# Kernel tuning notes

Hardware: AMD Instinct MI355X
Metric: run time of the kernel (lower is better)

## Reference

```python
import jax, jax.numpy as jnp
import numpy as np
import math

H = 128  # hidden_dim
RADIUS = 30.0


def _lin(x, w, b):
    return x @ w + b


def _masked_softmax(logits, mask):
    return jax.nn.softmax(jnp.where(mask, logits, -1e9), axis=-1)


def setup_inputs() -> dict:
    key = jax.random.key(0)
    ks = iter(jax.random.split(key, 64))

    def p(shape, s=0.02):
        return (jax.random.normal(next(ks), shape, jnp.float32) * s)

    B, N, T, M, L = 2, 48, 24, 192, 20
    inp = {
        'agents_state': jax.random.normal(next(ks), (B, N, T, 5), jnp.float32),
        'agents_mask': jnp.ones((B, N, T), jnp.float32),
        'map_polylines': jax.random.normal(next(ks), (B, M, L, 2), jnp.float32),
        'map_poly_mask': jnp.ones((B, M), jnp.float32),
        'map_poly_type': jax.random.randint(next(ks), (B, M), 0, 4),
        'map_tl_status': jax.random.randint(next(ks), (B, M), 0, 8),
        'map_on_route': jax.random.randint(next(ks), (B, M), 0, 2),
        # AgentStateEncoder
        'ae_w0': p((5, H)), 'ae_b0': p((H,)), 'ae_w1': p((H, H)), 'ae_b1': p((H,)),
        'ae_w2': p((H, H)), 'ae_b2': p((H,)),
        # MapPolylineNodeEncoder point_mlp
        'mp_w0': p((2, H)), 'mp_b0': p((H,)), 'mp_w1': p((H, H)), 'mp_b1': p((H,)),
        'type_emb': p((4, H)), 'tl_emb': p((8, H)), 'route_emb': p((2, H)),
        'mo_w0': p((H, H)), 'mo_b0': p((H,)), 'mo_w1': p((H, H)), 'mo_b1': p((H,)),
        # map_rel_mlp (3 -> H -> 1)
        'mr_w0': p((3, H)), 'mr_b0': p((H,)), 'mr_w1': p((H, 1)), 'mr_b1': p((1,)),
        # nbr_rel_mlp (5 -> H -> 1)
        'nr_w0': p((5, H)), 'nr_b0': p((H,)), 'nr_w1': p((H, 1)), 'nr_b1': p((1,)),
        # tau_out (3H -> H -> 64)
        'to_w0': p((3 * H, H)), 'to_b0': p((H,)), 'to_w1': p((H, 64)), 'to_b1': p((64,)),
    }
    return inp


def reference(agents_state, agents_mask, map_polylines, map_poly_mask,
              map_poly_type, map_tl_status, map_on_route,
              ae_w0, ae_b0, ae_w1, ae_b1, ae_w2, ae_b2,
              mp_w0, mp_b0, mp_w1, mp_b1, type_emb, tl_emb, route_emb,
              mo_w0, mo_b0, mo_w1, mo_b1,
              mr_w0, mr_b0, mr_w1, mr_b1,
              nr_w0, nr_b0, nr_w1, nr_b1,
              to_w0, to_b0, to_w1, to_b1):
    B, N, T, _ = agents_state.shape
    a_mask = agents_mask > 0.5
    a_feat = agents_state[..., :5]

    # --- MapPolylineNodeEncoder ---
    m = map_poly_mask > 0.5
    h = jax.nn.relu(_lin(jax.nn.relu(_lin(map_polylines, mp_w0, mp_b0)), mp_w1, mp_b1))  # B,M,L,H
    h = h.max(axis=2)  # B,M,H
    pt = jnp.clip(map_poly_type, 0, type_emb.shape[0] - 1)
    tl = jnp.clip(map_tl_status, 0, tl_emb.shape[0] - 1)
    rt = jnp.clip(map_on_route, 0, route_emb.shape[0] - 1)
    h = h + type_emb[pt] + tl_emb[tl] + route_emb[rt]
    h = _lin(jax.nn.relu(_lin(h, mo_w0, mo_b0)), mo_w1, mo_b1)
    map_node = h * m[..., None].astype(h.dtype)  # B,M,D
    map_center = map_polylines.mean(axis=2)  # B,M,2

    # --- AgentStateEncoder ---
    a = jax.nn.relu(_lin(a_feat, ae_w0, ae_b0))
    a = jax.nn.relu(_lin(a, ae_w1, ae_b1))
    a_emb = _lin(a, ae_w2, ae_b2) * a_mask[..., None].astype(a.dtype)  # B,N,T,D

    # --- map cross-attention with relative-position bias ---
    agent_pos = a_feat[..., 0:2]
    rel = map_center[:, None, None, :, :] - agent_pos[:, :, :, None, :]  # B,N,T,M,2
    dist = jnp.linalg.norm(rel, axis=-1, keepdims=True)
    rel_feat = jnp.concatenate([rel, dist], axis=-1)  # B,N,T,M,3
    rel_score = _lin(jax.nn.relu(_lin(rel_feat, mr_w0, mr_b0)), mr_w1, mr_b1)[..., 0]  # B,N,T,M
    dot = jnp.einsum('bntd,bmd->bntm', a_emb, map_node) / math.sqrt(map_node.shape[-1])
    attn = _masked_softmax(dot + rel_score, m[:, None, None, :])
    map_ctx = jnp.einsum('bntm,bmd->bntd', attn, map_node)

    # --- neighbor graph attention ---
    pos = a_feat[..., 0:2]
    vel = a_feat[..., 3:5]
    rel_pos = jnp.transpose(pos[:, :, None] - pos[:, None, :], (0, 1, 3, 2, 4))  # B,N,T,N,2
    rel_vel = jnp.transpose(vel[:, :, None] - vel[:, None, :], (0, 1, 3, 2, 4))
    dist_ij = jnp.linalg.norm(rel_pos, axis=-1, keepdims=True)  # B,N,T,N,1
    rel_ij = jnp.concatenate([rel_pos, rel_vel, dist_ij], axis=-1)  # B,N,T,N,5
    nbr_score = _lin(jax.nn.relu(_lin(rel_ij, nr_w0, nr_b0)), nr_w1, nr_b1)[..., 0]  # B,N,T,N

    valid_i = a_mask[..., None]  # B,N,T,1
    valid_j = jnp.transpose(a_mask, (0, 2, 1))[:, None, :, :]  # B,1,T,N
    radius_ok = dist_ij[..., 0] <= RADIUS
    not_self = ~jnp.eye(N, dtype=bool)[None, :, None, :]  # 1,N,1,N
    nbr_mask = valid_i & valid_j & radius_ok & not_self

    dot_n = jnp.einsum('bntd,bjtd->bntj', a_emb, a_emb) / math.sqrt(a_emb.shape[-1])
    w_n = _masked_softmax(dot_n + nbr_score, nbr_mask)  # B,N,T,N
    nbr_ctx = jnp.einsum('bntj,bjtd->bntd', w_n, a_emb)

    tau = jnp.concatenate([a_emb, map_ctx, nbr_ctx], axis=-1)
    tau = _lin(jax.nn.relu(_lin(tau, to_w0, to_b0)), to_w1, to_b1)
    tau = tau * a_mask[..., None].astype(tau.dtype)
    return tau, map_ctx, nbr_ctx
```

## Files before the change

kernel.cpp:

```cpp
#include <hip/hip_runtime.h>
#include <math.h>

#define HH 128
#define BB 2
#define NN 48
#define TT 24
#define MM 192
#define LL 20
#define NT (BB*NN*TT)
#define RSQRT_H 0.08838834764831845f
#define RADIUS_C 30.0f

struct P {
    const float *astate, *amask, *polylines, *poly_mask;
    const int *ptype, *tlst, *route;
    const float *ae_w0,*ae_b0,*ae_w1,*ae_b1,*ae_w2,*ae_b2;
    const float *mp_w0,*mp_b0,*mp_w1,*mp_b1;
    const float *type_emb,*tl_emb,*route_emb;
    const float *mo_w0,*mo_b0,*mo_w1,*mo_b1;
    const float *mr_w0,*mr_b0,*mr_w1,*mr_b1;
    const float *nr_w0,*nr_b0,*nr_w1,*nr_b1;
    const float *to_w0,*to_b0,*to_w1,*to_b1;
    float *tau,*map_ctx,*nbr_ctx;
    float *a_emb,*map_node,*map_nodeT,*map_center;
};

struct SME { float pts[LL*2]; float h1[LL][HH]; float mx[2][HH]; float hb[HH]; float pr[2][HH]; float hb2[HH]; };
struct SAG { float xin[4][5]; float h1[4][HH]; float h2[4][HH]; float p1[2][4][HH]; };

struct SF {
    float4 aq4L[HH];
    float  mctx[4][HH];
    float  nctx[4][HH];
    float  pc[2][4][HH];
    union {
        struct {
            float  mnL[16][MM];
            float4 w4L[HH];
            float  w1L[HH];
            float  lg[4][MM];
            float4 p4L[MM];
            float  invL[4];
        } m;
        struct {
            float  pjL[NN][8];
            float4 wAL[HH];
            float4 wBL[HH];
            float  sPL[4][4][NN];
            float  dPL[4][4][NN];
            float  lgN[4][NN];
            float4 pN[NN];
        } n;
        struct {
            float  xinT[3*HH][4];
            float  h1T[HH][4];
        } t;
    } u;
};

__device__ void do_map_enc(const P& p, SME& s, int bm) {
    int tid = threadIdx.x, pp = tid >> 7, c = tid & 127;
    if (tid < LL*2) s.pts[tid] = p.polylines[(size_t)bm*LL*2 + tid];
    __syncthreads();
    {
        float w0x = p.mp_w0[c], w0y = p.mp_w0[HH + c], b0 = p.mp_b0[c];
        #pragma unroll
        for (int i = 0; i < 10; ++i) {
            int pt_ = pp + 2*i;
            s.h1[pt_][c] = fmaxf(fmaf(s.pts[2*pt_], w0x, fmaf(s.pts[2*pt_+1], w0y, b0)), 0.f);
        }
    }
    if (tid < 2) {
        float sum = 0.f;
        for (int q = 0; q < LL; ++q) sum += s.pts[2*q + tid];
        p.map_center[bm*2 + tid] = sum * (1.0f / LL);
    }
    __syncthreads();
    {
        float acc[10];
        float b1 = p.mp_b1[c];
        #pragma unroll
        for (int i = 0; i < 10; ++i) acc[i] = b1;
        for (int k = 0; k < HH; ++k) {
            float wv = p.mp_w1[k*HH + c];
            #pragma unroll
            for (int i = 0; i < 10; ++i) acc[i] = fmaf(s.h1[pp + 2*i][k], wv, acc[i]);
        }
        float m10 = acc[0];
        #pragma unroll
        for (int i = 1; i < 10; ++i) m10 = fmaxf(m10, acc[i]);
        s.mx[pp][c] = m10;
    }
    __syncthreads();
    if (tid < HH) {
        float hm = fmaxf(fmaxf(s.mx[0][c], s.mx[1][c]), 0.f);
        int pt = p.ptype[bm]; pt = pt < 0 ? 0 : (pt > 3 ? 3 : pt);
        int tv = p.tlst[bm];  tv = tv < 0 ? 0 : (tv > 7 ? 7 : tv);
        int rv = p.route[bm]; rv = rv < 0 ? 0 : (rv > 1 ? 1 : rv);
        hm += p.type_emb[pt*HH + c] + p.tl_emb[tv*HH + c] + p.route_emb[rv*HH + c];
        s.hb[c] = hm;
    }
    __syncthreads();
    {
        float sum = 0.f;
        int k0 = pp*64;
        for (int k = k0; k < k0 + 64; ++k) sum = fmaf(s.hb[k], p.mo_w0[k*HH + c], sum);
        s.pr[pp][c] = sum;
    }
    __syncthreads();
    if (tid < HH) s.hb2[c] = fmaxf(s.pr[0][c] + s.pr[1][c] + p.mo_b0[c], 0.f);
    __syncthreads();
    {
        float sum = 0.f;
        int k0 = pp*64;
        for (int k = k0; k < k0 + 64; ++k) sum = fmaf(s.hb2[k], p.mo_w1[k*HH + c], sum);
        s.pr[pp][c] = sum;
    }
    __syncthreads();
    if (tid < HH) {
        float a3 = s.pr[0][c] + s.pr[1][c] + p.mo_b1[c];
        float mk = (p.poly_mask[bm] > 0.5f) ? 1.f : 0.f;
        float v = a3 * mk;
        p.map_node[(size_t)bm*HH + c] = v;
        int b = bm / MM, m = bm % MM;
        p.map_nodeT[((size_t)b*HH + c)*MM + m] = v;
    }
}

__device__ void do_agent_enc(const P& p, SAG& s, int r0) {
    int tid = threadIdx.x, h = tid >> 7, c = tid & 127;
    if (tid < 20) s.xin[tid/5][tid%5] = p.astate[(size_t)r0*5 + tid];
    __syncthreads();
    if (h == 0) {
        float b = p.ae_b0[c];
        float w[5];
        #pragma unroll
        for (int i = 0; i < 5; ++i) w[i] = p.ae_w0[i*HH + c];
        #pragma unroll
        for (int r = 0; r < 4; ++r) {
            float v = b;
            #pragma unroll
            for (int i = 0; i < 5; ++i) v = fmaf(s.xin[r][i], w[i], v);
            s.h1[r][c] = fmaxf(v, 0.f);
        }
    }
    __syncthreads();
    {
        float acc[4] = {0.f,0.f,0.f,0.f};
        int k0 = h*64;
        for (int k = k0; k < k0 + 64; ++k) {
            float wv = p.ae_w1[k*HH + c];
            #pragma unroll
            for (int r = 0; r < 4; ++r) acc[r] = fmaf(s.h1[r][k], wv, acc[r]);
        }
        #pragma unroll
        for (int r = 0; r < 4; ++r) s.p1[h][r][c] = acc[r];
    }
    __syncthreads();
    {
        #pragma unroll
        for (int rr = 0; rr < 2; ++rr) {
            int r = h*2 + rr;
            s.h2[r][c] = fmaxf(s.p1[0][r][c] + s.p1[1][r][c] + p.ae_b1[c], 0.f);
        }
    }
    __syncthreads();
    {
        float acc[4] = {0.f,0.f,0.f,0.f};
        int k0 = h*64;
        for (int k = k0; k < k0 + 64; ++k) {
            float wv = p.ae_w2[k*HH + c];
            #pragma unroll
            for (int r = 0; r < 4; ++r) acc[r] = fmaf(s.h2[r][k], wv, acc[r]);
        }
        #pragma unroll
        for (int r = 0; r < 4; ++r) s.p1[h][r][c] = acc[r];
    }
    __syncthreads();
    {
        #pragma unroll
        for (int rr = 0; rr < 2; ++rr) {
            int r = h*2 + rr;
            int row = r0 + r;
            p.a_emb[(size_t)row*HH + c] = (s.p1[0][r][c] + s.p1[1][r][c] + p.ae_b2[c]) * p.amask[row];
        }
    }
}

__global__ __launch_bounds__(256) void k_enc(P p) {
    __shared__ __align__(16) char smraw[(sizeof(SME) > sizeof(SAG)) ? sizeof(SME) : sizeof(SAG)];
    int task = blockIdx.x;
    if (task < BB*MM) do_map_enc(p, *(SME*)smraw, task);
    else              do_agent_enc(p, *(SAG*)smraw, (task - BB*MM)*4);
}

__global__ __launch_bounds__(256) void k_fat(P p) {
    __shared__ __align__(16) SF s;
    int task = blockIdx.x;
    int b    = task / (TT*12);
    int rem  = task % (TT*12);
    int t    = rem / 12;
    int n0   = (rem % 12) * 4;
    int tid  = threadIdx.x;

    int row0 = (b*NN + n0)*TT + t;

    for (int idx = tid; idx < 4*HH; idx += 256) {
        int r = idx >> 7, k = idx & 127;
        ((float*)&s.aq4L[k])[r] = p.a_emb[(size_t)(row0 + r*TT)*HH + k];
    }
    if (tid < HH) {
        int k = tid;
        s.u.m.w4L[k] = make_float4(p.mr_w0[k], p.mr_w0[HH+k], p.mr_w0[2*HH+k], p.mr_b0[k]);
        s.u.m.w1L[k] = p.mr_w1[k];
    }

    float rx[4], ry[4], rd[4];
    if (tid < MM) {
        float mcx = p.map_center[(b*MM + tid)*2];
        float mcy = p.map_center[(b*MM + tid)*2 + 1];
        #pragma unroll
        for (int r = 0; r < 4; ++r) {
            float px = p.astate[(size_t)(row0 + r*TT)*5];
            float py = p.astate[(size_t)(row0 + r*TT)*5 + 1];
            rx[r] = mcx - px; ry[r] = mcy - py;
            rd[r] = sqrtf(rx[r]*rx[r] + ry[r]*ry[r]);
        }
    }

    const float* mnT = p.map_nodeT + (size_t)b*HH*MM;
    float4 st[3];
    #pragma unroll
    for (int i = 0; i < 3; ++i) {
        int q = tid + 256*i;
        int kk = q / 48, mq = q % 48;
        st[i] = *(const float4*)(mnT + (size_t)kk*MM + mq*4);
    }
    float sacc[4] = {0.f,0.f,0.f,0.f};
    float dt4[4]  = {0.f,0.f,0.f,0.f};
    for (int ch = 0; ch < 8; ++ch) {
        __syncthreads();
        #pragma unroll
        for (int i = 0; i < 3; ++i) {
            int q = tid + 256*i;
            int kk = q / 48, mq = q % 48;
            *(float4*)&s.u.m.mnL[kk][mq*4] = st[i];
        }
        __syncthreads();
        if (ch < 7) {
            #pragma unroll
            for (int i = 0; i < 3; ++i) {
                int q = tid + 256*i;
                int kk = q / 48, mq = q % 48;
                st[i] = *(const float4*)(mnT + (size_t)(ch+1)*16*MM + (size_t)kk*MM + mq*4);
            }
        }
        if (tid < MM) {
            int k0 = ch*16;
            #pragma unroll
            for (int kk = 0; kk < 16; ++kk) {
                int k = k0 + kk;
                float4 w  = s.u.m.w4L[k];
                float  w1 = s.u.m.w1L[k];
                float4 aq = s.aq4L[k];
                float  mn = s.u.m.mnL[kk][tid];
                #pragma unroll
                for (int r = 0; r < 4; ++r) {
                    float hv = fmaf(rx[r], w.x, fmaf(ry[r], w.y, fmaf(rd[r], w.z, w.w)));
                    sacc[r] = fmaf(fmaxf(hv, 0.f), w1, sacc[r]);
                }
                dt4[0] = fmaf(aq.x, mn, dt4[0]);
                dt4[1] = fmaf(aq.y, mn, dt4[1]);
                dt4[2] = fmaf(aq.z, mn, dt4[2]);
                dt4[3] = fmaf(aq.w, mn, dt4[3]);
            }
        }
    }
    if (tid < MM) {
        float pm = p.poly_mask[b*MM + tid];
        float b1 = p.mr_b1[0];
        #pragma unroll
        for (int r = 0; r < 4; ++r) {
            float lgt = fmaf(dt4[r], RSQRT_H, sacc[r] + b1);
            s.u.m.lg[r][tid] = (pm > 0.5f) ? lgt : -1e9f;
        }
    }
    __syncthreads();

    {
        int r = tid >> 6, l = tid & 63;
        float v = fmaxf(fmaxf(s.u.m.lg[r][l], s.u.m.lg[r][l+64]), s.u.m.lg[r][l+128]);
        #pragma unroll
        for (int o = 32; o > 0; o >>= 1) v = fmaxf(v, __shfl_xor(v, o));
        float e0 = expf(s.u.m.lg[r][l] - v);
        float e1 = expf(s.u.m.lg[r][l+64] - v);
        float e2 = expf(s.u.m.lg[r][l+128] - v);
        s.u.m.lg[r][l] = e0; s.u.m.lg[r][l+64] = e1; s.u.m.lg[r][l+128] = e2;
        float sm = e0 + e1 + e2;
        #pragma unroll
        for (int o = 32; o > 0; o >>= 1) sm += __shfl_xor(sm, o);
        if (l == 0) s.u.m.invL[r] = 1.0f / sm;
    }
    __syncthreads();
    if (tid < MM) {
        s.u.m.p4L[tid] = make_float4(s.u.m.lg[0][tid]*s.u.m.invL[0], s.u.m.lg[1][tid]*s.u.m.invL[1],
                                     s.u.m.lg[2][tid]*s.u.m.invL[2], s.u.m.lg[3][tid]*s.u.m.invL[3]);
    }
    __syncthreads();

    {
        int half = tid >> 7, c = tid & 127;
        float a0=0.f, a1=0.f, a2=0.f, a3=0.f;
        const float* mnb = p.map_node + ((size_t)b*MM + half*96)*HH + c;
        for (int m = 0; m < 96; ++m) {
            float mv = mnb[(size_t)m*HH];
            float4 pp4 = s.u.m.p4L[half*96 + m];
            a0 = fmaf(pp4.x, mv, a0); a1 = fmaf(pp4.y, mv, a1);
            a2 = fmaf(pp4.z, mv, a2); a3 = fmaf(pp4.w, mv, a3);
        }
        s.pc[half][0][c]=a0; s.pc[half][1][c]=a1; s.pc[half][2][c]=a2; s.pc[half][3][c]=a3;
    }
    __syncthreads();
    for (int idx = tid; idx < 4*HH; idx += 256) {
        int r = idx >> 7, c = idx & 127;
        float v = s.pc[0][r][c] + s.pc[1][r][c];
        s.mctx[r][c] = v;
        p.map_ctx[(size_t)(row0 + r*TT)*HH + c] = v;
    }
    __syncthreads();

    if (tid < NN) {
        int rj = (b*NN + tid)*TT + t;
        s.u.n.pjL[tid][0] = p.astate[(size_t)rj*5];
        s.u.n.pjL[tid][1] = p.astate[(size_t)rj*5 + 1];
        s.u.n.pjL[tid][2] = p.astate[(size_t)rj*5 + 3];
        s.u.n.pjL[tid][3] = p.astate[(size_t)rj*5 + 4];
        s.u.n.pjL[tid][4] = p.amask[rj];
    }
    if (tid < HH) {
        int k = tid;
        s.u.n.wAL[k] = make_float4(p.nr_w0[k], p.nr_w0[HH+k], p.nr_w0[2*HH+k], p.nr_w0[3*HH+k]);
        s.u.n.wBL[k] = make_float4(p.nr_w0[4*HH+k], p.nr_b0[k], p.nr_w1[k], 0.f);
    }
    __syncthreads();

    {
        int j  = tid % 48;
        int kg = tid / 48;
        if (kg < 4) {
            float jx = s.u.n.pjL[j][0], jy = s.u.n.pjL[j][1];
            float jvx = s.u.n.pjL[j][2], jvy = s.u.n.pjL[j][3];
            float dx[4], dy[4], dvx[4], dvy[4], dd[4];
            #pragma unroll
            for (int r = 0; r < 4; ++r) {
                int ni = n0 + r;
                dx[r]  = s.u.n.pjL[ni][0] - jx;  dy[r]  = s.u.n.pjL[ni][1] - jy;
                dvx[r] = s.u.n.pjL[ni][2] - jvx; dvy[r] = s.u.n.pjL[ni][3] - jvy;
                dd[r]  = sqrtf(dx[r]*dx[r] + dy[r]*dy[r]);
            }
            const float* aj = p.a_emb + ((size_t)(b*NN + j)*TT + t)*HH;
            float sr[4]  = {0,0,0,0};
            float dtn[4] = {0,0,0,0};
            int k0 = kg*32;
            for (int kk = 0; kk < 32; ++kk) {
                int k = k0 + kk;
                float4 wa = s.u.n.wAL[k], wb = s.u.n.wBL[k];
                float4 aq = s.aq4L[k];
                float  av = aj[k];
                #pragma unroll
                for (int r = 0; r < 4; ++r) {
                    float hv = fmaf(dx[r], wa.x, fmaf(dy[r], wa.y,
                               fmaf(dvx[r], wa.z, fmaf(dvy[r], wa.w,
                               fmaf(dd[r], wb.x, wb.y)))));
                    sr[r] = fmaf(fmaxf(hv, 0.f), wb.z, sr[r]);
                }
                dtn[0] = fmaf(aq.x, av, dtn[0]); dtn[1] = fmaf(aq.y, av, dtn[1]);
                dtn[2] = fmaf(aq.z, av, dtn[2]); dtn[3] = fmaf(aq.w, av, dtn[3]);
            }
            #pragma unroll
            for (int r = 0; r < 4; ++r) { s.u.n.sPL[kg][r][j] = sr[r]; s.u.n.dPL[kg][r][j] = dtn[r]; }
        }
    }
    __syncthreads();

    {
        float b1 = p.nr_b1[0];
        for (int idx = tid; idx < 4*NN; idx += 256) {
            int r = idx / NN, jj = idx % NN;
            int ni = n0 + r;
            float ss  = s.u.n.sPL[0][r][jj] + s.u.n.sPL[1][r][jj] + s.u.n.sPL[2][r][jj] + s.u.n.sPL[3][r][jj] + b1;
            float do2 = s.u.n.dPL[0][r][jj] + s.u.n.dPL[1][r][jj] + s.u.n.dPL[2][r][jj] + s.u.n.dPL[3][r][jj];
            float ddx = s.u.n.pjL[ni][0] - s.u.n.pjL[jj][0];
            float ddy = s.u.n.pjL[ni][1] - s.u.n.pjL[jj][1];
            float dist = sqrtf(ddx*ddx + ddy*ddy);
            bool ok = (s.u.n.pjL[ni][4] > 0.5f) && (s.u.n.pjL[jj][4] > 0.5f) &&
                      (dist <= RADIUS_C) && (jj != ni);
            s.u.n.lgN[r][jj] = ok ? fmaf(do2, RSQRT_H, ss) : -1e9f;
        }
    }
    __syncthreads();

    {
        int r = tid >> 6, l = tid & 63;
        float v = (l < NN) ? s.u.n.lgN[r][l] : -3.4e38f;
        #pragma unroll
        for (int o = 32; o > 0; o >>= 1) v = fmaxf(v, __shfl_xor(v, o));
        float e = (l < NN) ? expf(s.u.n.lgN[r][l] - v) : 0.f;
        float sm = e;
        #pragma unroll
        for (int o = 32; o > 0; o >>= 1) sm += __shfl_xor(sm, o);
        if (l < NN) s.u.n.lgN[r][l] = e / sm;
    }
    __syncthreads();
    if (tid < NN) {
        s.u.n.pN[tid] = make_float4(s.u.n.lgN[0][tid], s.u.n.lgN[1][tid],
                                    s.u.n.lgN[2][tid], s.u.n.lgN[3][tid]);
    }
    __syncthreads();

    {
        int half = tid >> 7, c = tid & 127;
        float a0=0.f, a1=0.f, a2=0.f, a3=0.f;
        for (int jj = half*24; jj < half*24 + 24; ++jj) {
            float av = p.a_emb[((size_t)(b*NN + jj)*TT + t)*HH + c];
            float4 pp4 = s.u.n.pN[jj];
            a0 = fmaf(pp4.x, av, a0); a1 = fmaf(pp4.y, av, a1);
            a2 = fmaf(pp4.z, av, a2); a3 = fmaf(pp4.w, av, a3);
        }
        s.pc[half][0][c]=a0; s.pc[half][1][c]=a1; s.pc[half][2][c]=a2; s.pc[half][3][c]=a3;
    }
    __syncthreads();
    for (int idx = tid; idx < 4*HH; idx += 256) {
        int r = idx >> 7, c = idx & 127;
        float v = s.pc[0][r][c] + s.pc[1][r][c];
        s.nctx[r][c] = v;
        p.nbr_ctx[(size_t)(row0 + r*TT)*HH + c] = v;
    }
    __syncthreads();

    for (int idx = tid; idx < 4*HH; idx += 256) {
        int r = idx >> 7, k = idx & 127;
        s.u.t.xinT[k][r]        = ((float*)&s.aq4L[k])[r];
        s.u.t.xinT[HH + k][r]   = s.mctx[r][k];
        s.u.t.xinT[2*HH + k][r] = s.nctx[r][k];
    }
    __syncthreads();
    {
        int c = tid & 127, h = tid >> 7;
        float acc[4] = {0,0,0,0};
        for (int k = h*192; k < h*192 + 192; ++k) {
            float wv = p.to_w0[k*HH + c];
            float4 xa = *(const float4*)&s.u.t.xinT[k][0];
            acc[0]=fmaf(xa.x,wv,acc[0]); acc[1]=fmaf(xa.y,wv,acc[1]);
            acc[2]=fmaf(xa.z,wv,acc[2]); acc[3]=fmaf(xa.w,wv,acc[3]);
        }
        #pragma unroll
        for (int r = 0; r < 4; ++r) s.pc[h][r][c] = acc[r];
    }
    __syncthreads();
    for (int idx = tid; idx < 4*HH; idx += 256) {
        int r = idx >> 7, k = idx & 127;
        s.u.t.h1T[k][r] = fmaxf(s.pc[0][r][k] + s.pc[1][r][k] + p.to_b0[k], 0.f);
    }
    __syncthreads();
    {
        int r = tid >> 6, c2 = tid & 63;
        float acc = p.to_b1[c2];
        for (int k = 0; k < HH; ++k)
            acc = fmaf(s.u.t.h1T[k][r], p.to_w1[k*64 + c2], acc);
        p.tau[(size_t)(row0 + r*TT)*64 + c2] = acc * p.amask[row0 + r*TT];
    }
}

extern "C" void kernel_launch(void* const* d_in, const int* in_sizes, int n_in,
                              void* d_out, int out_size, void* d_ws, size_t ws_size,
                              hipStream_t stream)
{
    P p;
    p.astate    = (const float*)d_in[0];
    p.amask     = (const float*)d_in[1];
    p.polylines = (const float*)d_in[2];
    p.poly_mask = (const float*)d_in[3];
    p.ptype     = (const int*)d_in[4];
    p.tlst      = (const int*)d_in[5];
    p.route     = (const int*)d_in[6];
    p.ae_w0 = (const float*)d_in[7];  p.ae_b0 = (const float*)d_in[8];
    p.ae_w1 = (const float*)d_in[9];  p.ae_b1 = (const float*)d_in[10];
    p.ae_w2 = (const float*)d_in[11]; p.ae_b2 = (const float*)d_in[12];
    p.mp_w0 = (const float*)d_in[13]; p.mp_b0 = (const float*)d_in[14];
    p.mp_w1 = (const float*)d_in[15]; p.mp_b1 = (const float*)d_in[16];
    p.type_emb  = (const float*)d_in[17];
    p.tl_emb    = (const float*)d_in[18];
    p.route_emb = (const float*)d_in[19];
    p.mo_w0 = (const float*)d_in[20]; p.mo_b0 = (const float*)d_in[21];
    p.mo_w1 = (const float*)d_in[22]; p.mo_b1 = (const float*)d_in[23];
    p.mr_w0 = (const float*)d_in[24]; p.mr_b0 = (const float*)d_in[25];
    p.mr_w1 = (const float*)d_in[26]; p.mr_b1 = (const float*)d_in[27];
    p.nr_w0 = (const float*)d_in[28]; p.nr_b0 = (const float*)d_in[29];
    p.nr_w1 = (const float*)d_in[30]; p.nr_b1 = (const float*)d_in[31];
    p.to_w0 = (const float*)d_in[32]; p.to_b0 = (const float*)d_in[33];
    p.to_w1 = (const float*)d_in[34]; p.to_b1 = (const float*)d_in[35];

    p.tau     = (float*)d_out;
    p.map_ctx = (float*)d_out + (size_t)NT*64;
    p.nbr_ctx = p.map_ctx + (size_t)NT*HH;

    float* ws    = (float*)d_ws;
    p.a_emb      = ws;
    p.map_node   = p.a_emb + (size_t)NT*HH;
    p.map_nodeT  = p.map_node + (size_t)BB*MM*HH;
    p.map_center = p.map_nodeT + (size_t)BB*MM*HH;

    k_enc<<<BB*MM + NT/4, 256, 0, stream>>>(p);
    k_fat<<<BB*TT*12,     256, 0, stream>>>(p);
}
```

Measured before the change: 187.9 us.

## Split agent encoder to two rows per block and simplify map-score and output stages

Agent encoding now handles two rows per block instead of four, doubling the block count. The map MLP's hidden buffer is transposed so each thread reads contiguous points. The map-attention loop drops its staged LDS copy of map_nodeT and reads coalesced columns straight from global memory, which removes eight barriers. The tau stage now splits the K dimension across both thread halves for two of its rows, while the other two rows run serially. Together these trade extra blocks and global reads for fewer barriers and more parallelism, though the uneven tau tail and the uncached global reads could offset some of that.

```diff
diff --git a/kernel.cpp b/kernel.cpp
--- a/kernel.cpp
+++ b/kernel.cpp
@@ -25,8 +25,8 @@
     float *a_emb,*map_node,*map_nodeT,*map_center;
 };
 
-struct SME { float pts[LL*2]; float h1[LL][HH]; float mx[2][HH]; float hb[HH]; float pr[2][HH]; float hb2[HH]; };
-struct SAG { float xin[4][5]; float h1[4][HH]; float h2[4][HH]; float p1[2][4][HH]; };
+struct SME { float pts[LL*2]; float h1T[HH][LL]; float mx[2][HH]; float hb[HH]; float pr[2][HH]; float hb2[HH]; };
+struct SAG { float xin[2][5]; float h1[2][HH]; float h2[2][HH]; float p1[2][2][HH]; };
 
 struct SF {
     float4 aq4L[HH];
@@ -35,7 +35,6 @@
     float  pc[2][4][HH];
     union {
         struct {
-            float  mnL[16][MM];
             float4 w4L[HH];
             float  w1L[HH];
             float  lg[4][MM];
@@ -52,8 +51,8 @@
             float4 pN[NN];
         } n;
         struct {
-            float  xinT[3*HH][4];
-            float  h1T[HH][4];
+            float4 xinT[3*HH];
+            float4 h1T[HH];
         } t;
     } u;
 };
@@ -66,8 +65,8 @@
         float w0x = p.mp_w0[c], w0y = p.mp_w0[HH + c], b0 = p.mp_b0[c];
         #pragma unroll
         for (int i = 0; i < 10; ++i) {
-            int pt_ = pp + 2*i;
-            s.h1[pt_][c] = fmaxf(fmaf(s.pts[2*pt_], w0x, fmaf(s.pts[2*pt_+1], w0y, b0)), 0.f);
+            int pt_ = pp*10 + i;
+            s.h1T[c][pt_] = fmaxf(fmaf(s.pts[2*pt_], w0x, fmaf(s.pts[2*pt_+1], w0y, b0)), 0.f);
         }
     }
     if (tid < 2) {
@@ -83,8 +82,9 @@
         for (int i = 0; i < 10; ++i) acc[i] = b1;
         for (int k = 0; k < HH; ++k) {
             float wv = p.mp_w1[k*HH + c];
+            const float* hrow = &s.h1T[k][pp*10];
             #pragma unroll
-            for (int i = 0; i < 10; ++i) acc[i] = fmaf(s.h1[pp + 2*i][k], wv, acc[i]);
+            for (int i = 0; i < 10; ++i) acc[i] = fmaf(hrow[i], wv, acc[i]);
         }
         float m10 = acc[0];
         #pragma unroll
@@ -129,7 +129,7 @@
 
 __device__ void do_agent_enc(const P& p, SAG& s, int r0) {
     int tid = threadIdx.x, h = tid >> 7, c = tid & 127;
-    if (tid < 20) s.xin[tid/5][tid%5] = p.astate[(size_t)r0*5 + tid];
+    if (tid < 10) s.xin[tid/5][tid%5] = p.astate[(size_t)r0*5 + tid];
     __syncthreads();
     if (h == 0) {
         float b = p.ae_b0[c];
@@ -137,7 +137,7 @@
         #pragma unroll
         for (int i = 0; i < 5; ++i) w[i] = p.ae_w0[i*HH + c];
         #pragma unroll
-        for (int r = 0; r < 4; ++r) {
+        for (int r = 0; r < 2; ++r) {
             float v = b;
             #pragma unroll
             for (int i = 0; i < 5; ++i) v = fmaf(s.xin[r][i], w[i], v);
@@ -146,44 +146,36 @@
     }
     __syncthreads();
     {
-        float acc[4] = {0.f,0.f,0.f,0.f};
+        float a0 = 0.f, a1 = 0.f;
         int k0 = h*64;
         for (int k = k0; k < k0 + 64; ++k) {
             float wv = p.ae_w1[k*HH + c];
-            #pragma unroll
-            for (int r = 0; r < 4; ++r) acc[r] = fmaf(s.h1[r][k], wv, acc[r]);
-        }
-        #pragma unroll
-        for (int r = 0; r < 4; ++r) s.p1[h][r][c] = acc[r];
-    }
-    __syncthreads();
-    {
-        #pragma unroll
-        for (int rr = 0; rr < 2; ++rr) {
-            int r = h*2 + rr;
-            s.h2[r][c] = fmaxf(s.p1[0][r][c] + s.p1[1][r][c] + p.ae_b1[c], 0.f);
-        }
-    }
-    __syncthreads();
-    {
-        float acc[4] = {0.f,0.f,0.f,0.f};
+            a0 = fmaf(s.h1[0][k], wv, a0);
+            a1 = fmaf(s.h1[1][k], wv, a1);
+        }
+        s.p1[h][0][c] = a0; s.p1[h][1][c] = a1;
+    }
+    __syncthreads();
+    {
+        int r = h;
+        s.h2[r][c] = fmaxf(s.p1[0][r][c] + s.p1[1][r][c] + p.ae_b1[c], 0.f);
+    }
+    __syncthreads();
+    {
+        float a0 = 0.f, a1 = 0.f;
         int k0 = h*64;
         for (int k = k0; k < k0 + 64; ++k) {
             float wv = p.ae_w2[k*HH + c];
-            #pragma unroll
-            for (int r = 0; r < 4; ++r) acc[r] = fmaf(s.h2[r][k], wv, acc[r]);
-        }
-        #pragma unroll
-        for (int r = 0; r < 4; ++r) s.p1[h][r][c] = acc[r];
-    }
-    __syncthreads();
-    {
-        #pragma unroll
-        for (int rr = 0; rr < 2; ++rr) {
-            int r = h*2 + rr;
-            int row = r0 + r;
-            p.a_emb[(size_t)row*HH + c] = (s.p1[0][r][c] + s.p1[1][r][c] + p.ae_b2[c]) * p.amask[row];
-        }
+            a0 = fmaf(s.h2[0][k], wv, a0);
+            a1 = fmaf(s.h2[1][k], wv, a1);
+        }
+        s.p1[h][0][c] = a0; s.p1[h][1][c] = a1;
+    }
+    __syncthreads();
+    {
+        int r = h;
+        int row = r0 + r;
+        p.a_emb[(size_t)row*HH + c] = (s.p1[0][r][c] + s.p1[1][r][c] + p.ae_b2[c]) * p.amask[row];
     }
 }
 
@@ -191,7 +183,7 @@
     __shared__ __align__(16) char smraw[(sizeof(SME) > sizeof(SAG)) ? sizeof(SME) : sizeof(SAG)];
     int task = blockIdx.x;
     if (task < BB*MM) do_map_enc(p, *(SME*)smraw, task);
-    else              do_agent_enc(p, *(SAG*)smraw, (task - BB*MM)*4);
+    else              do_agent_enc(p, *(SAG*)smraw, (task - BB*MM)*2);
 }
 
 __global__ __launch_bounds__(256) void k_fat(P p) {
@@ -227,43 +219,22 @@
             rd[r] = sqrtf(rx[r]*rx[r] + ry[r]*ry[r]);
         }
     }
-
-    const float* mnT = p.map_nodeT + (size_t)b*HH*MM;
-    float4 st[3];
-    #pragma unroll
-    for (int i = 0; i < 3; ++i) {
-        int q = tid + 256*i;
-        int kk = q / 48, mq = q % 48;
-        st[i] = *(const float4*)(mnT + (size_t)kk*MM + mq*4);
-    }
-    float sacc[4] = {0.f,0.f,0.f,0.f};
-    float dt4[4]  = {0.f,0.f,0.f,0.f};
-    for (int ch = 0; ch < 8; ++ch) {
-        __syncthreads();
-        #pragma unroll
-        for (int i = 0; i < 3; ++i) {
-            int q = tid + 256*i;
-            int kk = q / 48, mq = q % 48;
-            *(float4*)&s.u.m.mnL[kk][mq*4] = st[i];
-        }
-        __syncthreads();
-        if (ch < 7) {
+    __syncthreads();
+
+    if (tid < MM) {
+        const float* mnc = p.map_nodeT + (size_t)b*HH*MM + tid;
+        float sacc[4] = {0.f,0.f,0.f,0.f};
+        float dt4[4]  = {0.f,0.f,0.f,0.f};
+        const float4* w1q4 = (const float4*)s.u.m.w1L;
+        for (int kq = 0; kq < HH/4; ++kq) {
+            float4 w1q = w1q4[kq];
             #pragma unroll
-            for (int i = 0; i < 3; ++i) {
-                int q = tid + 256*i;
-                int kk = q / 48, mq = q % 48;
-                st[i] = *(const float4*)(mnT + (size_t)(ch+1)*16*MM + (size_t)kk*MM + mq*4);
-            }
-        }
-        if (tid < MM) {
-            int k0 = ch*16;
-            #pragma unroll
-            for (int kk = 0; kk < 16; ++kk) {
-                int k = k0 + kk;
+            for (int j = 0; j < 4; ++j) {
+                int k = kq*4 + j;
                 float4 w  = s.u.m.w4L[k];
-                float  w1 = s.u.m.w1L[k];
                 float4 aq = s.aq4L[k];
-                float  mn = s.u.m.mnL[kk][tid];
+                float  w1 = ((const float*)&w1q)[j];
+                float  mn = mnc[(size_t)k*MM];
                 #pragma unroll
                 for (int r = 0; r < 4; ++r) {
                     float hv = fmaf(rx[r], w.x, fmaf(ry[r], w.y, fmaf(rd[r], w.z, w.w)));
@@ -275,8 +246,6 @@
                 dt4[3] = fmaf(aq.w, mn, dt4[3]);
             }
         }
-    }
-    if (tid < MM) {
         float pm = p.poly_mask[b*MM + tid];
         float b1 = p.mr_b1[0];
         #pragma unroll
@@ -359,9 +328,10 @@
                 dd[r]  = sqrtf(dx[r]*dx[r] + dy[r]*dy[r]);
             }
             const float* aj = p.a_emb + ((size_t)(b*NN + j)*TT + t)*HH;
-            float sr[4]  = {0,0,0,0};
-            float dtn[4] = {0,0,0,0};
+            float sr[4]  = {0.f,0.f,0.f,0.f};
+            float dtn[4] = {0.f,0.f,0.f,0.f};
             int k0 = kg*32;
+            #pragma unroll 4
             for (int kk = 0; kk < 32; ++kk) {
                 int k = k0 + kk;
                 float4 wa = s.u.n.wAL[k], wb = s.u.n.wBL[k];
@@ -438,11 +408,16 @@
     }
     __syncthreads();
 
-    for (int idx = tid; idx < 4*HH; idx += 256) {
-        int r = idx >> 7, k = idx & 127;
-        s.u.t.xinT[k][r]        = ((float*)&s.aq4L[k])[r];
-        s.u.t.xinT[HH + k][r]   = s.mctx[r][k];
-        s.u.t.xinT[2*HH + k][r] = s.nctx[r][k];
+    for (int idx = tid; idx < 3*HH; idx += 256) {
+        if (idx < HH) {
+            s.u.t.xinT[idx] = s.aq4L[idx];
+        } else if (idx < 2*HH) {
+            int k = idx - HH;
+            s.u.t.xinT[idx] = make_float4(s.mctx[0][k], s.mctx[1][k], s.mctx[2][k], s.mctx[3][k]);
+        } else {
+            int k = idx - 2*HH;
+            s.u.t.xinT[idx] = make_float4(s.nctx[0][k], s.nctx[1][k], s.nctx[2][k], s.nctx[3][k]);
+        }
     }
     __syncthreads();
     {
@@ -450,9 +425,9 @@
         float acc[4] = {0,0,0,0};
         for (int k = h*192; k < h*192 + 192; ++k) {
             float wv = p.to_w0[k*HH + c];
-            float4 xa = *(const float4*)&s.u.t.xinT[k][0];
-            acc[0]=fmaf(xa.x,wv,acc[0]); acc[1]=fmaf(xa.y,wv,acc[1]);
-            acc[2]=fmaf(xa.z,wv,acc[2]); acc[3]=fmaf(xa.w,wv,acc[3]);
+            float4 x4 = s.u.t.xinT[k];
+            acc[0]=fmaf(x4.x,wv,acc[0]); acc[1]=fmaf(x4.y,wv,acc[1]);
+            acc[2]=fmaf(x4.z,wv,acc[2]); acc[3]=fmaf(x4.w,wv,acc[3]);
         }
         #pragma unroll
         for (int r = 0; r < 4; ++r) s.pc[h][r][c] = acc[r];
@@ -460,15 +435,33 @@
     __syncthreads();
     for (int idx = tid; idx < 4*HH; idx += 256) {
         int r = idx >> 7, k = idx & 127;
-        s.u.t.h1T[k][r] = fmaxf(s.pc[0][r][k] + s.pc[1][r][k] + p.to_b0[k], 0.f);
-    }
-    __syncthreads();
-    {
+        ((float*)&s.u.t.h1T[k])[r] = fmaxf(s.pc[0][r][k] + s.pc[1][r][k] + p.to_b0[k], 0.f);
+    }
+    __syncthreads();
+    {
+        int kh = tid >> 7, rc = tid & 127;
+        int r = rc >> 6, c2 = rc & 63;
+        float acc = 0.f;
+        for (int k = kh*64; k < kh*64 + 64; ++k)
+            acc = fmaf(((const float*)&s.u.t.h1T[k])[r], p.to_w1[k*64 + c2], acc);
+        s.pc[kh][r][c2] = acc;
+    }
+    __syncthreads();
+    if (tid < 128) {
         int r = tid >> 6, c2 = tid & 63;
-        float acc = p.to_b1[c2];
+        int row = row0 + r*TT;
+        float v = (s.pc[0][r][c2] + s.pc[1][r][c2] + p.to_b1[c2]) * p.amask[row];
+        p.tau[(size_t)row*64 + c2] = v;
+    }
+    __syncthreads();
+    if (tid < 128) {
+        int r = 2 + (tid >> 6), c2 = tid & 63;
+        int row = row0 + r*TT;
+        float acc = 0.f;
         for (int k = 0; k < HH; ++k)
-            acc = fmaf(s.u.t.h1T[k][r], p.to_w1[k*64 + c2], acc);
-        p.tau[(size_t)(row0 + r*TT)*64 + c2] = acc * p.amask[row0 + r*TT];
+            acc = fmaf(((const float*)&s.u.t.h1T[k])[r], p.to_w1[k*64 + c2], acc);
+        float v = (acc + p.to_b1[c2]) * p.amask[row];
+        p.tau[(size_t)row*64 + c2] = v;
     }
 }
 
@@ -511,6 +504,6 @@
     p.map_nodeT  = p.map_node + (size_t)BB*MM*HH;
     p.map_center = p.map_nodeT + (size_t)BB*MM*HH;
 
-    k_enc<<<BB*MM + NT/4, 256, 0, stream>>>(p);
+    k_enc<<<BB*MM + NT/2, 256, 0, stream>>>(p);
     k_fat<<<BB*TT*12,     256, 0, stream>>>(p);
 }
```

Result: no change. 184.2 us (-2.0%).
